# Kernel tuning notes

Hardware: AMD Instinct MI355X
Metric: run time of the kernel (lower is better)

Reference implementation:

```python
import jax, jax.numpy as jnp
import numpy as np

B, N, F, P, E, EMB = 32, 51, 4, 137, 408, 32


def _gcn_norm(edge_index, num_nodes):
    # add self loops, symmetric normalization D^-1/2 (A+I) D^-1/2 (PyG gcn_norm)
    loops = jnp.arange(num_nodes, dtype=edge_index.dtype)
    src = jnp.concatenate([edge_index[0], loops])
    dst = jnp.concatenate([edge_index[1], loops])
    w = jnp.ones(src.shape[0], dtype=jnp.float32)
    deg = jnp.zeros((num_nodes,), jnp.float32).at[dst].add(w)
    dinv = jnp.where(deg > 0, 1.0 / jnp.sqrt(deg), 0.0)
    norm = dinv[src] * w * dinv[dst]
    return src, dst, norm


def _gcn_conv(x, W, b, src, dst, norm, num_nodes):
    # x: [B, P, N, Fin] -> [B, P, N, Fout]; linear first, then normalized aggregation
    xw = jnp.einsum('bpnf,fe->bpne', x, W)
    msg = xw[:, :, src, :] * norm[None, None, :, None]
    out = jnp.zeros(xw.shape[:2] + (num_nodes, W.shape[1]), xw.dtype).at[:, :, dst, :].add(msg)
    return out + b


def _forward(x, edge_index, conv_z_w, conv_z_b, conv_r_w, conv_r_b, conv_h_w, conv_h_b,
             lin_z_w, lin_z_b, lin_r_w, lin_r_b, lin_h_w, lin_h_b, attention,
             lin1_w, lin1_b, lin2_w, lin2_b, lin3_w, lin3_b):
    num_nodes = x.shape[1]
    xt = jnp.transpose(x, (0, 3, 1, 2))  # [B, P, N, F] -- periods as a batch dim
    src, dst, norm = _gcn_norm(edge_index, num_nodes)
    # A3TGCN2 never updates H across periods (H stays None -> zeros), so all 137
    # TGCN2 cell evaluations are independent and can be vectorized over P.
    cz = _gcn_conv(xt, conv_z_w, conv_z_b, src, dst, norm, num_nodes)
    ch = _gcn_conv(xt, conv_h_w, conv_h_b, src, dst, norm, num_nodes)
    zeros_h = jnp.zeros_like(cz)
    # Z = sigmoid(lin_z([conv_z(x), H])) with H = 0
    Z = jax.nn.sigmoid(jnp.concatenate([cz, zeros_h], axis=-1) @ lin_z_w + lin_z_b)
    # R gate multiplies H (= 0) so it has no effect on the output; omitted (DCE-equivalent).
    # H_tilde = tanh(lin_h([conv_h(x), H * R])) with H = 0
    Ht = jnp.tanh(jnp.concatenate([ch, zeros_h], axis=-1) @ lin_h_w + lin_h_b)
    Hp = (1.0 - Z) * Ht  # Z*H + (1-Z)*H_tilde with H = 0 -> [B, P, N, EMB]
    probs = jax.nn.softmax(attention)
    h = jnp.einsum('p,bpne->bne', probs, Hp)  # attention-weighted accumulation
    h = jax.nn.relu(h)
    # dropout(0.2) is identity in eval mode
    h = jax.nn.relu(h @ lin1_w + lin1_b)
    h = h @ lin2_w + lin2_b            # [B, N, 1]
    h = h.reshape(-1, num_nodes)       # [B, N]
    h = jax.nn.sigmoid(h @ lin3_w + lin3_b)  # [B, 1]
    return h.reshape(-1)


def setup_inputs() -> dict:
    key = jax.random.key(0)
    ks = jax.random.split(key, 16)
    def rn(k, shape, scale=0.1):
        return jax.random.normal(k, shape, dtype=jnp.float32) * scale
    return {
        'x': jax.random.normal(ks[0], (B, N, F, P), dtype=jnp.float32),
        'edge_index': jax.random.randint(ks[1], (2, E), 0, N, dtype=jnp.int32),
        'conv_z_w': rn(ks[2], (F, EMB)), 'conv_z_b': jnp.zeros((EMB,), jnp.float32),
        'conv_r_w': rn(ks[3], (F, EMB)), 'conv_r_b': jnp.zeros((EMB,), jnp.float32),
        'conv_h_w': rn(ks[4], (F, EMB)), 'conv_h_b': jnp.zeros((EMB,), jnp.float32),
        'lin_z_w': rn(ks[5], (2 * EMB, EMB)), 'lin_z_b': jnp.zeros((EMB,), jnp.float32),
        'lin_r_w': rn(ks[6], (2 * EMB, EMB)), 'lin_r_b': jnp.zeros((EMB,), jnp.float32),
        'lin_h_w': rn(ks[7], (2 * EMB, EMB)), 'lin_h_b': jnp.zeros((EMB,), jnp.float32),
        'attention': jax.random.uniform(ks[8], (P,), dtype=jnp.float32),
        'lin1_w': rn(ks[9], (EMB, 32)), 'lin1_b': jnp.zeros((32,), jnp.float32),
        'lin2_w': rn(ks[10], (32, 1)), 'lin2_b': jnp.zeros((1,), jnp.float32),
        'lin3_w': rn(ks[11], (N, 1)), 'lin3_b': jnp.zeros((1,), jnp.float32),
    }


def reference(x, edge_index, conv_z_w, conv_z_b, conv_r_w, conv_r_b, conv_h_w, conv_h_b,
              lin_z_w, lin_z_b, lin_r_w, lin_r_b, lin_h_w, lin_h_b, attention,
              lin1_w, lin1_b, lin2_w, lin2_b, lin3_w, lin3_b):
    return _forward(x, edge_index, conv_z_w, conv_z_b, conv_r_w, conv_r_b, conv_h_w, conv_h_b,
                    lin_z_w, lin_z_b, lin_r_w, lin_r_b, lin_h_w, lin_h_b, attention,
                    lin1_w, lin1_b, lin2_w, lin2_b, lin3_w, lin3_b)
```

## Files before the change

kernel.cpp:

```cpp
#include <hip/hip_runtime.h>
#include <hip/hip_bf16.h>

#define NND 51
#define FIN 4
#define PDIM 137
#define EMB 32
#define EE 408
#define BD 32
#define PC 5
#define NCH 28
#define NE (NND*EMB)

#define WS_AMP   0
#define WS_PROBS 2608
#define WS_WU    2752
#define WS_BEFF  3008
#define WS_CNT   3072
#define WS_H     3104

#define OFF_AS   0
#define OFF_XS   2604
#define OFF_AG   3624
#define OFF_WU   4644
#define OFF_BE   4900
#define OFF_PR   4964
#define OFF_FLAG 4972
#define SM_N     4976
#define H_HS     0
#define H_W1     1632
#define H_B1     2656
#define H_W2     2688
#define H_W3     2720
#define H_WS     2772

__global__ __launch_bounds__(256) void setup_kernel(
    const int* __restrict__ ei, const float* __restrict__ att,
    const float* __restrict__ Wz, const float* __restrict__ bz,
    const float* __restrict__ Wh, const float* __restrict__ bh,
    const float* __restrict__ Uz, const float* __restrict__ bz2,
    const float* __restrict__ Uh, const float* __restrict__ bh2,
    float* __restrict__ ws)
{
    int t = threadIdx.x, blk = blockIdx.x;
    if (blk > 0) {
        float4* dst = (float4*)(ws + WS_CNT);
        const int n4 = (32 + BD * NE) / 4;
        float4 z = make_float4(0.f, 0.f, 0.f, 0.f);
        for (int i = (blk - 1) * 256 + t; i < n4; i += 7 * 256) dst[i] = z;
        return;
    }
    __shared__ float deg[NND], dinv[NND];
    __shared__ float Am[2604];
    __shared__ float Us[2][EMB * EMB];
    __shared__ float Ws2[2][FIN * EMB];
    __shared__ float atts[PDIM];
    __shared__ float inv_sum;
    for (int i = t; i < 2604; i += 256) Am[i] = 0.0f;
    if (t < NND) deg[t] = 0.0f;
    for (int i = t; i < EMB * EMB; i += 256) { Us[0][i] = Uz[i]; Us[1][i] = Uh[i]; }
    if (t < FIN * EMB) { Ws2[0][t] = Wz[t]; Ws2[1][t] = Wh[t]; }
    if (t < PDIM) atts[t] = att[t];
    __syncthreads();
    for (int e = t; e < EE; e += 256) atomicAdd(&deg[ei[EE + e]], 1.0f);
    __syncthreads();
    if (t < NND) dinv[t] = rsqrtf(deg[t] + 1.0f);
    __syncthreads();
    for (int e = t; e < EE; e += 256) {
        int s = ei[e], d = ei[EE + e];
        atomicAdd(&Am[d * NND + s], dinv[s] * dinv[d]);
    }
    {
        int g = t >> 7, f = (t >> 5) & 3, e = t & 31;
        float a = 0.0f;
        for (int k = 0; k < EMB; k++) a += Ws2[g][f * EMB + k] * Us[g][k * EMB + e];
        ws[WS_WU + t] = a;
    }
    if (t < 64) {
        int g = t >> 5, e = t & 31;
        const float* bb = g ? bh : bz;
        const float* b2 = g ? bh2 : bz2;
        float a = b2[e];
        for (int k = 0; k < EMB; k++) a += bb[k] * Us[g][k * EMB + e];
        ws[WS_BEFF + t] = a;
    }
    __syncthreads();
    if (t < NND) Am[t * 52] += dinv[t] * dinv[t];
    if (t == 0) {
        float m = -1e30f;
        for (int p = 0; p < PDIM; p++) m = fmaxf(m, atts[p]);
        float s = 0.0f;
        for (int p = 0; p < PDIM; p++) { float v = __expf(atts[p] - m); atts[p] = v; s += v; }
        inv_sum = 1.0f / s;
    }
    __syncthreads();
    for (int i = t; i < 2604; i += 256) ws[WS_AMP + i] = Am[i];
    if (t < PDIM) ws[WS_PROBS + t] = atts[t] * inv_sum;
}

__global__ __launch_bounds__(256) void fused_kernel(
    const float* __restrict__ x, float* __restrict__ ws,
    float* __restrict__ h, const float* __restrict__ W1,
    const float* __restrict__ b1, const float* __restrict__ w2,
    const float* __restrict__ b2, const float* __restrict__ w3,
    const float* __restrict__ b3, float* __restrict__ out)
{
    __shared__ __align__(16) float sm[SM_N];
    int t = threadIdx.x;
    int b = blockIdx.y;
    int c = blockIdx.x;
    int p0 = c * PC;
    int npp = min(PC, PDIM - p0);

    for (int i = t; i < 651; i += 256)
        ((float4*)(sm + OFF_AS))[i] = ((const float4*)(ws + WS_AMP))[i];
    sm[OFF_WU + t] = ws[WS_WU + t];
    if (t < 64) sm[OFF_BE + t] = ws[WS_BEFF + t];
    if (t < npp) sm[OFF_PR + t] = ws[WS_PROBS + p0 + t];
    if (t < NND * FIN) {
        int n = t >> 2, f = t & 3;
        const float* xp = &x[((b * NND + n) * FIN + f) * PDIM + p0];
        for (int pp = 0; pp < npp; pp++) sm[OFF_XS + (pp * NND + n) * 4 + f] = xp[pp];
    }
    __syncthreads();

    int e = t & 31, r = t >> 5;
    float wuz[4], wuh[4];
    #pragma unroll
    for (int f = 0; f < 4; f++) {
        wuz[f] = sm[OFF_WU + f * EMB + e];
        wuh[f] = sm[OFF_WU + 128 + f * EMB + e];
    }
    float bez = sm[OFF_BE + e], beh = sm[OFF_BE + 32 + e];

    if (t < NND * PC) {
        int pp = t / NND, d = t - pp * NND;
        if (pp < npp) {
            const float*  Ad = sm + OFF_AS + d * NND;
            const float4* xr = (const float4*)(sm + OFF_XS) + pp * NND;
            float4 acc = make_float4(0.f, 0.f, 0.f, 0.f);
            #pragma unroll 3
            for (int s = 0; s < NND; s++) {
                float a = Ad[s]; float4 xv = xr[s];
                acc.x += a * xv.x; acc.y += a * xv.y;
                acc.z += a * xv.z; acc.w += a * xv.w;
            }
            ((float4*)(sm + OFF_AG))[pp * NND + d] = acc;
        }
    }
    __syncthreads();

    float hacc[7] = {0, 0, 0, 0, 0, 0, 0};
    for (int pp = 0; pp < npp; pp++) {
        float pr = sm[OFF_PR + pp];
        #pragma unroll
        for (int k = 0; k < 7; k++) {
            int d = r + 8 * k;
            if (d < NND) {
                float4 ag = ((const float4*)(sm + OFF_AG))[pp * NND + d];
                float az = bez + ag.x * wuz[0] + ag.y * wuz[1] + ag.z * wuz[2] + ag.w * wuz[3];
                float ah = beh + ag.x * wuh[0] + ag.y * wuh[1] + ag.z * wuh[2] + ag.w * wuh[3];
                float Z  = 1.0f / (1.0f + __expf(-az));
                float Ht = 2.0f / (1.0f + __expf(-2.0f * ah)) - 1.0f;
                hacc[k] += pr * (1.0f - Z) * Ht;
            }
        }
    }
    float* dst = &h[b * NE];
    #pragma unroll
    for (int k = 0; k < 7; k++) {
        int d = r + 8 * k;
        if (d < NND) atomicAdd(&dst[d * EMB + e], hacc[k]);
    }

    __syncthreads();
    if (t == 0) {
        __threadfence();
        int old = atomicAdd((int*)(ws + WS_CNT) + b, 1);
        *(int*)(sm + OFF_FLAG) = (old == NCH - 1);
    }
    __syncthreads();
    if (!*(int*)(sm + OFF_FLAG)) return;

    for (int i = t; i < NE; i += 256) {
        float v = __hip_atomic_load(&h[b * NE + i], __ATOMIC_RELAXED,
                                    __HIP_MEMORY_SCOPE_AGENT);
        sm[H_HS + i] = fmaxf(v, 0.0f);
    }
    for (int i = t; i < EMB * EMB; i += 256) sm[H_W1 + i] = W1[i];
    if (t < EMB) { sm[H_B1 + t] = b1[t]; sm[H_W2 + t] = w2[t]; }
    if (t < NND) sm[H_W3 + t] = w3[t];
    __syncthreads();
    float acc = 0.0f;
    for (int i = t; i < NE; i += 256) {
        int d = i >> 5, ee = i & 31;
        float a = sm[H_B1 + ee];
        const float* hr = sm + H_HS + d * EMB;
        #pragma unroll
        for (int k = 0; k < EMB; k++) a += hr[k] * sm[H_W1 + k * EMB + ee];
        a = fmaxf(a, 0.0f);
        acc += sm[H_W3 + d] * sm[H_W2 + ee] * a;
    }
    #pragma unroll
    for (int off = 32; off > 0; off >>= 1) acc += __shfl_down(acc, off);
    if ((t & 63) == 0) sm[H_WS + (t >> 6)] = acc;
    __syncthreads();
    if (t == 0) {
        float s = sm[H_WS] + sm[H_WS + 1] + sm[H_WS + 2] + sm[H_WS + 3];
        float s3 = 0.0f;
        for (int d = 0; d < NND; d++) s3 += sm[H_W3 + d];
        float v = s + b2[0] * s3 + b3[0];
        out[b] = 1.0f / (1.0f + __expf(-v));
    }
}

extern "C" void kernel_launch(void* const* d_in, const int* in_sizes, int n_in,
                              void* d_out, int out_size, void* d_ws, size_t ws_size,
                              hipStream_t stream) {
    const float* x         = (const float*)d_in[0];
    const int*   ei        = (const int*)d_in[1];
    const float* conv_z_w  = (const float*)d_in[2];
    const float* conv_z_b  = (const float*)d_in[3];
    const float* conv_h_w  = (const float*)d_in[6];
    const float* conv_h_b  = (const float*)d_in[7];
    const float* lin_z_w   = (const float*)d_in[8];
    const float* lin_z_b   = (const float*)d_in[9];
    const float* lin_h_w   = (const float*)d_in[12];
    const float* lin_h_b   = (const float*)d_in[13];
    const float* attention = (const float*)d_in[14];
    const float* lin1_w    = (const float*)d_in[15];
    const float* lin1_b    = (const float*)d_in[16];
    const float* lin2_w    = (const float*)d_in[17];
    const float* lin2_b    = (const float*)d_in[18];
    const float* lin3_w    = (const float*)d_in[19];
    const float* lin3_b    = (const float*)d_in[20];

    float* ws = (float*)d_ws;
    float* h  = ws + WS_H;

    hipLaunchKernelGGL(setup_kernel, dim3(8), dim3(256), 0, stream,
                       ei, attention, conv_z_w, conv_z_b, conv_h_w, conv_h_b,
                       lin_z_w, lin_z_b, lin_h_w, lin_h_b, ws);
    hipLaunchKernelGGL(fused_kernel, dim3(NCH, BD), dim3(256), 0, stream,
                       x, ws, h, lin1_w, lin1_b, lin2_w, lin2_b,
                       lin3_w, lin3_b, (float*)d_out);
}
```

Baseline: 136.3 us.

## Split fused kernel into main and separate head kernel, drop last-block counter

Replaces the atomic-counter last-block-done pattern, where the final chunk block for each batch ran the MLP head, with a separate head kernel launched after the main aggregation kernel. This removes the threadfence, the counter atomic and the extra barriers from every main block. In exchange it adds a third kernel launch and its launch gap, and the head runs as a separate 32-block pass. The setup kernel still zeros the now-unused counter area.

Result: faster. 131.7 us (-3.4%).

```diff
diff --git a/kernel.cpp b/kernel.cpp
--- a/kernel.cpp
+++ b/kernel.cpp
@@ -24,14 +24,7 @@
 #define OFF_WU   4644
 #define OFF_BE   4900
 #define OFF_PR   4964
-#define OFF_FLAG 4972
-#define SM_N     4976
-#define H_HS     0
-#define H_W1     1632
-#define H_B1     2656
-#define H_W2     2688
-#define H_W3     2720
-#define H_WS     2772
+#define SM_N     4972
 
 __global__ __launch_bounds__(256) void setup_kernel(
     const int* __restrict__ ei, const float* __restrict__ att,
@@ -97,12 +90,9 @@
     if (t < PDIM) ws[WS_PROBS + t] = atts[t] * inv_sum;
 }
 
-__global__ __launch_bounds__(256) void fused_kernel(
-    const float* __restrict__ x, float* __restrict__ ws,
-    float* __restrict__ h, const float* __restrict__ W1,
-    const float* __restrict__ b1, const float* __restrict__ w2,
-    const float* __restrict__ b2, const float* __restrict__ w3,
-    const float* __restrict__ b3, float* __restrict__ out)
+__global__ __launch_bounds__(256) void main_kernel(
+    const float* __restrict__ x, const float* __restrict__ ws,
+    float* __restrict__ h)
 {
     __shared__ __align__(16) float sm[SM_N];
     int t = threadIdx.x;
@@ -171,43 +161,43 @@
         int d = r + 8 * k;
         if (d < NND) atomicAdd(&dst[d * EMB + e], hacc[k]);
     }
-
-    __syncthreads();
-    if (t == 0) {
-        __threadfence();
-        int old = atomicAdd((int*)(ws + WS_CNT) + b, 1);
-        *(int*)(sm + OFF_FLAG) = (old == NCH - 1);
-    }
-    __syncthreads();
-    if (!*(int*)(sm + OFF_FLAG)) return;
-
-    for (int i = t; i < NE; i += 256) {
-        float v = __hip_atomic_load(&h[b * NE + i], __ATOMIC_RELAXED,
-                                    __HIP_MEMORY_SCOPE_AGENT);
-        sm[H_HS + i] = fmaxf(v, 0.0f);
-    }
-    for (int i = t; i < EMB * EMB; i += 256) sm[H_W1 + i] = W1[i];
-    if (t < EMB) { sm[H_B1 + t] = b1[t]; sm[H_W2 + t] = w2[t]; }
-    if (t < NND) sm[H_W3 + t] = w3[t];
+}
+
+__global__ __launch_bounds__(256) void head_kernel(
+    const float* __restrict__ h, const float* __restrict__ W1,
+    const float* __restrict__ b1, const float* __restrict__ w2,
+    const float* __restrict__ b2, const float* __restrict__ w3,
+    const float* __restrict__ b3, float* __restrict__ out)
+{
+    __shared__ float hs[NE];
+    __shared__ float W1s[EMB * EMB];
+    __shared__ float b1s[EMB], w2s[EMB];
+    __shared__ float w3s[NND];
+    __shared__ float wsum[4];
+    int t = threadIdx.x, b = blockIdx.x;
+    for (int i = t; i < NE; i += 256) hs[i] = fmaxf(h[b * NE + i], 0.0f);
+    for (int i = t; i < EMB * EMB; i += 256) W1s[i] = W1[i];
+    if (t < EMB) { b1s[t] = b1[t]; w2s[t] = w2[t]; }
+    if (t < NND) w3s[t] = w3[t];
     __syncthreads();
     float acc = 0.0f;
     for (int i = t; i < NE; i += 256) {
-        int d = i >> 5, ee = i & 31;
-        float a = sm[H_B1 + ee];
-        const float* hr = sm + H_HS + d * EMB;
+        int d = i >> 5, e = i & 31;
+        float a = b1s[e];
+        const float* hr = &hs[d * EMB];
         #pragma unroll
-        for (int k = 0; k < EMB; k++) a += hr[k] * sm[H_W1 + k * EMB + ee];
+        for (int k = 0; k < EMB; k++) a += hr[k] * W1s[k * EMB + e];
         a = fmaxf(a, 0.0f);
-        acc += sm[H_W3 + d] * sm[H_W2 + ee] * a;
+        acc += w3s[d] * w2s[e] * a;
     }
     #pragma unroll
     for (int off = 32; off > 0; off >>= 1) acc += __shfl_down(acc, off);
-    if ((t & 63) == 0) sm[H_WS + (t >> 6)] = acc;
+    if ((t & 63) == 0) wsum[t >> 6] = acc;
     __syncthreads();
     if (t == 0) {
-        float s = sm[H_WS] + sm[H_WS + 1] + sm[H_WS + 2] + sm[H_WS + 3];
+        float s = wsum[0] + wsum[1] + wsum[2] + wsum[3];
         float s3 = 0.0f;
-        for (int d = 0; d < NND; d++) s3 += sm[H_W3 + d];
+        for (int d = 0; d < NND; d++) s3 += w3s[d];
         float v = s + b2[0] * s3 + b3[0];
         out[b] = 1.0f / (1.0f + __expf(-v));
     }
@@ -240,7 +230,9 @@
     hipLaunchKernelGGL(setup_kernel, dim3(8), dim3(256), 0, stream,
                        ei, attention, conv_z_w, conv_z_b, conv_h_w, conv_h_b,
                        lin_z_w, lin_z_b, lin_h_w, lin_h_b, ws);
-    hipLaunchKernelGGL(fused_kernel, dim3(NCH, BD), dim3(256), 0, stream,
-                       x, ws, h, lin1_w, lin1_b, lin2_w, lin2_b,
-                       lin3_w, lin3_b, (float*)d_out);
-}
+    hipLaunchKernelGGL(main_kernel, dim3(NCH, BD), dim3(256), 0, stream,
+                       x, ws, h);
+    hipLaunchKernelGGL(head_kernel, dim3(BD), dim3(256), 0, stream,
+                       h, lin1_w, lin1_b, lin2_w, lin2_b, lin3_w, lin3_b,
+                       (float*)d_out);
+}
```
